# Performance work log

Measured on AMD Instinct MI355X. Metric: run time of the kernel, lower is better.

## Reference

```python
import jax, jax.numpy as jnp
import numpy as np

HEADS = 8

def _flatten(x, s1, s2):
    # 'b c (h s1) (w s2) -> b (h w) (s1 s2 c)'
    b, c, H, W = x.shape
    h, w = H // s1, W // s2
    x = x.reshape(b, c, h, s1, w, s2).transpose(0, 2, 4, 3, 5, 1)
    return x.reshape(b, h * w, s1 * s2 * c)

def _unflatten(x, h, w, s1, s2):
    # 'b (h w) (s1 s2 c) -> b c (h s1) (w s2)'
    b, n, e = x.shape
    c = e // (s1 * s2)
    x = x.reshape(b, h, w, s1, s2, c).transpose(0, 5, 1, 3, 2, 4)
    return x.reshape(b, c, h * s1, w * s2)

def _attn(x_detail, x_context, wq, bq, wk, bk, wv, bv, wo, bo):
    E = x_detail.shape[-1]
    d = E // HEADS
    scale = d ** -0.5
    def split(t):
        b, n, _ = t.shape
        return t.reshape(b, n, HEADS, d).transpose(0, 2, 1, 3)  # b h n d
    q = split(x_context @ wq.T + bq)
    k = split(x_detail @ wk.T + bk)
    v = split(x_detail @ wv.T + bv)
    att = jax.nn.softmax(jnp.einsum('bhqd,bhkd->bhqk', q, k) * scale, axis=-1)
    out = jnp.einsum('bhqk,bhkd->bhqd', att, v)
    b, h, n, _ = out.shape
    out = out.transpose(0, 2, 1, 3).reshape(b, n, E)
    return out @ wo.T + bo

def setup_inputs() -> dict:
    key = jax.random.key(0)
    ks = iter(jax.random.split(key, 64))
    inp = {}
    xshapes = [(16, 96, 56, 56), (16, 192, 28, 28), (16, 384, 14, 14), (16, 768, 7, 7)]
    names = ['x00', 'x10', 'x20', 'x30']
    for nm, sh in zip(names, xshapes):
        inp[nm + '_detail'] = jax.random.normal(next(ks), sh, dtype=jnp.float32)
        inp[nm + '_context'] = jax.random.normal(next(ks), sh, dtype=jnp.float32)
    embs = [384, 192, 384, 768]
    for i, E in enumerate(embs):
        for p in ['q', 'k', 'v', 'o']:
            inp[f'w{p}{i}'] = jax.random.normal(next(ks), (E, E), dtype=jnp.float32) * 0.02
            inp[f'b{p}{i}'] = jnp.zeros((E,), dtype=jnp.float32)
    return inp

def reference(x00_detail, x00_context, x10_detail, x10_context,
              x20_detail, x20_context, x30_detail, x30_context,
              wq0, bq0, wk0, bk0, wv0, bv0, wo0, bo0,
              wq1, bq1, wk1, bk1, wv1, bv1, wo1, bo1,
              wq2, bq2, wk2, bk2, wv2, bv2, wo2, bo2,
              wq3, bq3, wk3, bk3, wv3, bv3, wo3, bo3):
    # scale 0: 56x56 with 2x2 patching -> 784 tokens, emb 384
    o0 = x00_detail + _unflatten(
        _attn(_flatten(x00_detail, 2, 2), _flatten(x00_context, 2, 2),
              wq0, bq0, wk0, bk0, wv0, bv0, wo0, bo0), 28, 28, 2, 2)
    # scale 1: 28x28 -> 784 tokens, emb 192
    o1 = x10_detail + _unflatten(
        _attn(_flatten(x10_detail, 1, 1), _flatten(x10_context, 1, 1),
              wq1, bq1, wk1, bk1, wv1, bv1, wo1, bo1), 28, 28, 1, 1)
    # scale 2: 14x14 -> 196 tokens, emb 384
    o2 = x20_detail + _unflatten(
        _attn(_flatten(x20_detail, 1, 1), _flatten(x20_context, 1, 1),
              wq2, bq2, wk2, bk2, wv2, bv2, wo2, bo2), 14, 14, 1, 1)
    # scale 3: 7x7 -> 49 tokens, emb 768
    o3 = x30_detail + _unflatten(
        _attn(_flatten(x30_detail, 1, 1), _flatten(x30_context, 1, 1),
              wq3, bq3, wk3, bk3, wv3, bv3, wo3, bo3), 7, 7, 1, 1)
    return (o0, o1, o2, o3)
```

## Files before the change

### kernel.cpp

```cpp
#include <hip/hip_runtime.h>
#include <hip/hip_bf16.h>
#include <cstdint>
#include <cstddef>
#include <cmath>

typedef unsigned short bf16u;
typedef float f32x4 __attribute__((ext_vector_type(4)));
typedef short frag8 __attribute__((ext_vector_type(8)));

typedef __attribute__((address_space(1))) uint32_t u32g;
typedef __attribute__((address_space(3))) uint32_t u32l;

__device__ __forceinline__ void async_cp16(const bf16u* g, bf16u* l) {
    __builtin_amdgcn_global_load_lds((u32g*)g, (u32l*)l, 16, 0, 0);
}

__device__ __forceinline__ bf16u f2bf(float f) {
    union { float f; uint32_t u; } v; v.f = f;
    uint32_t u = v.u;
    return (bf16u)((u + 0x7fffu + ((u >> 16) & 1u)) >> 16);
}

__device__ __forceinline__ uint32_t pk2bf(float a, float b) {
    __hip_bfloat162 h = __float22bfloat162_rn(make_float2(a, b));
    union { __hip_bfloat162 h; uint32_t u; } c; c.h = h; return c.u;
}

__device__ __forceinline__ int vperm(int n) {
    return (n & ~63) | ((n & 15) << 2) | ((n >> 4) & 3);
}

static constexpr int cN[4]   = {784, 784, 196, 49};
static constexpr int cE[4]   = {384, 192, 384, 768};
static constexpr int cM[4]   = {12544, 12544, 3136, 784};
static constexpr int cC[4]   = {96, 192, 384, 768};
static constexpr int cH[4]   = {56, 28, 14, 7};
static constexpr int cS[4]   = {2, 1, 1, 1};
static constexpr int cWt[4]  = {28, 28, 14, 7};

static constexpr size_t xoff[4] = {0, 4816896, 7225344, 8429568};
static constexpr size_t voff[4] = {0, 6815744, 10223616, 12320768};
static constexpr size_t woff[4] = {0, 589824, 737280, 1327104};

__device__ __constant__ float qsc[4] = {0.20823509f, 0.29448888f, 0.20823509f, 0.14724444f};

static constexpr int hStart[5] = {0, 588, 735, 813, 1401};
static constexpr int oStart[5]  = {0,294,369,411,999};

static constexpr int fStart[9] = {0,4800,9600,12000,14400,15744,17088,17856,18624};
static constexpr int wCum[17]  = {0,72,144,216,288,306,324,342,360,432,504,576,648,936,1224,1512,1800};
static constexpr int fNtn[4] = {25, 25, 7, 2};
static constexpr int fNtc[4] = {3, 6, 12, 24};
static constexpr int fSp[4]  = {4, 1, 1, 1};

struct BiasP { const float* p[16]; };
struct PrepP { const float* x[8]; const float* w[16]; };
struct OunfP { const float* xd[4]; };

__global__ __launch_bounds__(256) void prep(PrepP pp, bf16u* __restrict__ Xd,
                                            bf16u* __restrict__ Xc, bf16u* __restrict__ Wb) {
    int blk = blockIdx.x, tid = threadIdx.x;
    if (blk < 18624) {
        __shared__ float tile[32][33];
        int seg = 0;
        while (seg < 7 && blk >= fStart[seg + 1]) seg++;
        int s = seg >> 1, which = seg & 1;
        int l = blk - fStart[seg];
        int ntn = fNtn[s], ntc = fNtc[s], sp = fSp[s];
        int nt = l % ntn; l /= ntn;
        int ctl = l % ntc; l /= ntc;
        int spi = l % sp; int b = l / sp;
        int sv = cS[s];
        int s1i = spi / sv, s2i = spi % sv;
        int C = cC[s], H = cH[s], Wd = cH[s], N = cN[s], E2 = cE[s], Wt = cWt[s];
        const float* x = pp.x[s * 2 + which];
        bf16u* dst = (which ? Xc : Xd) + xoff[s];
        int tx = tid & 31, ty = tid >> 5;
        int n0 = nt * 32, c0 = ctl * 32;
#pragma unroll
        for (int rr = 0; rr < 4; ++rr) {
            int c = c0 + rr * 8 + ty;
            int n = n0 + tx;
            if (n < N) {
                int hh = (n / Wt) * sv + s1i;
                int ww = (n % Wt) * sv + s2i;
                tile[rr * 8 + ty][tx] = x[((size_t)(b * C + c) * H + hh) * Wd + ww];
            }
        }
        __syncthreads();
        int ebase = (s1i * sv + s2i) * C + c0;
#pragma unroll
        for (int rr = 0; rr < 4; ++rr) {
            int n = n0 + rr * 8 + ty;
            if (n < N)
                dst[((size_t)b * N + n) * E2 + ebase + tx] = f2bf(tile[tx][rr * 8 + ty]);
        }
    } else {
        int wb = blk - 18624;
        int m2 = 0;
        while (m2 < 15 && wb >= wCum[m2 + 1]) m2++;
        int s = m2 >> 2, mi = m2 & 3;
        size_t e2 = (size_t)cE[s] * cE[s];
        size_t base = (size_t)(wb - wCum[m2]) * 2048 + tid * 8;
        const float* src = pp.w[m2];
        bf16u* dst = Wb + woff[s] + mi * e2 + base;
        float4 a = *(const float4*)(src + base);
        float4 c = *(const float4*)(src + base + 4);
        bf16u o[8] = {f2bf(a.x), f2bf(a.y), f2bf(a.z), f2bf(a.w),
                      f2bf(c.x), f2bf(c.y), f2bf(c.z), f2bf(c.w)};
        *(frag8*)dst = *(frag8*)o;
    }
}

__device__ __forceinline__ void gemm_q_h(const bf16u* __restrict__ A, const bf16u* __restrict__ W,
                                         const float* __restrict__ bias,
                                         int M, int E, int mTile, int eTile, float oscale,
                                         bf16u* __restrict__ outB, bf16u* sm) {
    bf16u* As = sm;
    bf16u* Bs = sm + 2048;
    int tid = threadIdx.x, wave = tid >> 6, lane = tid & 63;
    int mbase = mTile * 64, ebase = eTile * 128;
    int wm = (wave & 1) * 32, wn = (wave >> 1) * 64;
    f32x4 acc[2][4] = {};
    int srow = tid >> 2, sch = (tid & 3) * 8;
    int K = E;
    int m = mbase + srow; if (m >= M) m = M - 1;
    const bf16u* Ag  = A + (size_t)m * K + sch;
    const bf16u* Wg0 = W + (size_t)(ebase + srow) * K + sch;
    const bf16u* Wg1 = W + (size_t)(ebase + srow + 64) * K + sch;
    int la = (lane & 15) * 32 + (lane >> 4) * 8;

    for (int k0 = 0; k0 < K; k0 += 32) {
        async_cp16(Ag + k0, As + tid * 8);
        async_cp16(Wg0 + k0, Bs + tid * 8);
        async_cp16(Wg1 + k0, Bs + 2048 + tid * 8);
        __syncthreads();
        frag8 af[2], bfr[4];
#pragma unroll
        for (int i = 0; i < 2; ++i)
            af[i] = *(const frag8*)(As + (wm + i * 16) * 32 + la);
#pragma unroll
        for (int j = 0; j < 4; ++j)
            bfr[j] = *(const frag8*)(Bs + (wn + j * 16) * 32 + la);
#pragma unroll
        for (int i = 0; i < 2; ++i)
#pragma unroll
            for (int j = 0; j < 4; ++j)
                acc[i][j] = __builtin_amdgcn_mfma_f32_16x16x32_bf16(af[i], bfr[j], acc[i][j], 0, 0, 0);
        __syncthreads();
    }

    int mrow = lane & 15, quad = lane >> 4;
#pragma unroll
    for (int mt = 0; mt < 2; ++mt) {
#pragma unroll
        for (int nt = 0; nt < 4; ++nt) {
            int col = ebase + wn + nt * 16 + mrow;
            float bv = bias[col];
            int rbase = mbase + wm + mt * 16 + quad * 4;
#pragma unroll
            for (int r = 0; r < 4; ++r) {
                int rowg = rbase + r;
                if (rowg >= M) continue;
                outB[(size_t)rowg * E + col] = f2bf((acc[mt][nt][r] + bv) * oscale);
            }
        }
    }
}

template<int NN, int DHt, int DHPt, int NJt>
__device__ __forceinline__ void gemm_kv_h(const bf16u* __restrict__ A, const bf16u* __restrict__ Wk,
                                          const bf16u* __restrict__ Wv,
                                          const float* __restrict__ bk, const float* __restrict__ bv,
                                          int M, int E, int mTile, int eTile,
                                          bf16u* __restrict__ Ko, bf16u* __restrict__ Vo, bf16u* sm) {
    bf16u* As = sm;
    bf16u* Ks = sm + 2048;
    bf16u* Vs = sm + 6144;
    int tid = threadIdx.x, wave = tid >> 6, lane = tid & 63;
    int mbase = mTile * 64, ebase = eTile * 128;
    int wm = (wave & 1) * 32, wn = (wave >> 1) * 64;
    f32x4 acck[2][4] = {};
    f32x4 accv[2][4] = {};
    int srow = tid >> 2, sch = (tid & 3) * 8;
    int Kd = E;
    int m = mbase + srow; if (m >= M) m = M - 1;
    const bf16u* Ag  = A + (size_t)m * Kd + sch;
    const bf16u* Kg0 = Wk + (size_t)(ebase + srow) * Kd + sch;
    const bf16u* Kg1 = Wk + (size_t)(ebase + srow + 64) * Kd + sch;
    const bf16u* Vg0 = Wv + (size_t)(ebase + srow) * Kd + sch;
    const bf16u* Vg1 = Wv + (size_t)(ebase + srow + 64) * Kd + sch;
    int la = (lane & 15) * 32 + (lane >> 4) * 8;

    for (int k0 = 0; k0 < Kd; k0 += 32) {
        async_cp16(Ag + k0, As + tid * 8);
        async_cp16(Kg0 + k0, Ks + tid * 8);
        async_cp16(Kg1 + k0, Ks + 2048 + tid * 8);
        async_cp16(Vg0 + k0, Vs + tid * 8);
        async_cp16(Vg1 + k0, Vs + 2048 + tid * 8);
        __syncthreads();
        frag8 af[2], bfr[4];
#pragma unroll
        for (int i = 0; i < 2; ++i)
            af[i] = *(const frag8*)(As + (wm + i * 16) * 32 + la);
#pragma unroll
        for (int j = 0; j < 4; ++j)
            bfr[j] = *(const frag8*)(Ks + (wn + j * 16) * 32 + la);
#pragma unroll
        for (int i = 0; i < 2; ++i)
#pragma unroll
            for (int j = 0; j < 4; ++j)
                acck[i][j] = __builtin_amdgcn_mfma_f32_16x16x32_bf16(af[i], bfr[j], acck[i][j], 0, 0, 0);
#pragma unroll
        for (int j = 0; j < 4; ++j)
            bfr[j] = *(const frag8*)(Vs + (wn + j * 16) * 32 + la);
#pragma unroll
        for (int i = 0; i < 2; ++i)
#pragma unroll
            for (int j = 0; j < 4; ++j)
                accv[i][j] = __builtin_amdgcn_mfma_f32_16x16x32_bf16(af[i], bfr[j], accv[i][j], 0, 0, 0);
        __syncthreads();
    }

    int mrow = lane & 15, quad = lane >> 4;
#pragma unroll
    for (int mt = 0; mt < 2; ++mt) {
#pragma unroll
        for (int nt = 0; nt < 4; ++nt) {
            int col = ebase + wn + nt * 16 + mrow;
            float bkc = bk[col];
            int rbase = mbase + wm + mt * 16 + quad * 4;
#pragma unroll
            for (int r = 0; r < 4; ++r) {
                int rowg = rbase + r;
                if (rowg >= M) continue;
                Ko[(size_t)rowg * E + col] = f2bf(acck[mt][nt][r] + bkc);
            }
        }
    }

    bf16u* vt = sm;
#pragma unroll
    for (int mt = 0; mt < 2; ++mt) {
#pragma unroll
        for (int nt = 0; nt < 4; ++nt) {
            int cl = wn + nt * 16 + mrow;
            float bvc = bv[ebase + cl];
            int rl0 = wm + mt * 16 + quad * 4;
#pragma unroll
            for (int r = 0; r < 4; ++r)
                vt[cl * 66 + rl0 + r] = f2bf(accv[mt][nt][r] + bvc);
        }
    }
    __syncthreads();
    {
        int rowg = mbase + lane;
        bool ok = rowg < M;
        int b2 = rowg / NN, n = rowg - b2 * NN;
        int vp = vperm(n);
        int c0 = wave * 32;
#pragma unroll
        for (int ci = 0; ci < 32; ++ci) {
            int c = c0 + ci;
            int colg = ebase + c;
            int hh = colg / DHt, d = colg - hh * DHt;
            if (ok)
                Vo[((size_t)(b2 * 8 + hh) * DHPt + d) * NJt + vp] = vt[c * 66 + lane];
        }
    }
}

__device__ __forceinline__ void gemm_q64_s1(const bf16u* __restrict__ A, const bf16u* __restrict__ W,
                                            const float* __restrict__ bias,
                                            int M, int E, int mTile, int eTile, float oscale,
                                            bf16u* __restrict__ outB, bf16u* sm) {
    bf16u* As = sm;
    bf16u* Bs = sm + 2048;
    int tid = threadIdx.x, wave = tid >> 6, lane = tid & 63;
    int mbase = mTile * 64, ebase = eTile * 64;
    int wm = (wave & 1) * 32, wn = (wave >> 1) * 32;
    f32x4 acc[2][2] = {};
    int srow = tid >> 2, sch = (tid & 3) * 8;
    int K = E;
    int m = mbase + srow; if (m >= M) m = M - 1;
    const bf16u* Ag = A + (size_t)m * K + sch;
    const bf16u* Wg = W + (size_t)(ebase + srow) * K + sch;
    int la = (lane & 15) * 32 + (lane >> 4) * 8;

    for (int k0 = 0; k0 < K; k0 += 32) {
        async_cp16(Ag + k0, As + tid * 8);
        async_cp16(Wg + k0, Bs + tid * 8);
        __syncthreads();
        frag8 af0 = *(const frag8*)(As + wm * 32 + la);
        frag8 af1 = *(const frag8*)(As + (wm + 16) * 32 + la);
        frag8 bf0 = *(const frag8*)(Bs + wn * 32 + la);
        frag8 bf1 = *(const frag8*)(Bs + (wn + 16) * 32 + la);
        acc[0][0] = __builtin_amdgcn_mfma_f32_16x16x32_bf16(af0, bf0, acc[0][0], 0, 0, 0);
        acc[0][1] = __builtin_amdgcn_mfma_f32_16x16x32_bf16(af0, bf1, acc[0][1], 0, 0, 0);
        acc[1][0] = __builtin_amdgcn_mfma_f32_16x16x32_bf16(af1, bf0, acc[1][0], 0, 0, 0);
        acc[1][1] = __builtin_amdgcn_mfma_f32_16x16x32_bf16(af1, bf1, acc[1][1], 0, 0, 0);
        __syncthreads();
    }

    int mrow = lane & 15, quad = lane >> 4;
#pragma unroll
    for (int mt = 0; mt < 2; ++mt) {
#pragma unroll
        for (int nt = 0; nt < 2; ++nt) {
            int col = ebase + wn + nt * 16 + mrow;
            float bv = bias[col];
            int rbase = mbase + wm + mt * 16 + quad * 4;
#pragma unroll
            for (int r = 0; r < 4; ++r) {
                int rowg = rbase + r;
                if (rowg >= M) continue;
                outB[(size_t)rowg * E + col] = f2bf((acc[mt][nt][r] + bv) * oscale);
            }
        }
    }
}

template<int NN, int DHt, int DHPt, int NJt>
__device__ __forceinline__ void gemm_kv64(const bf16u* __restrict__ A, const bf16u* __restrict__ Wk,
                                          const bf16u* __restrict__ Wv,
                                          const float* __restrict__ bk, const float* __restrict__ bv,
                                          int M, int E, int mTile, int eTile,
                                          bf16u* __restrict__ Ko, bf16u* __restrict__ Vo, bf16u* sm) {
    bf16u* As = sm;
    bf16u* Ks = sm + 2048;
    bf16u* Vs = sm + 4096;
    int tid = threadIdx.x, wave = tid >> 6, lane = tid & 63;
    int mbase = mTile * 64, ebase = eTile * 64;
    int wm = (wave & 1) * 32, wn = (wave >> 1) * 32;
    f32x4 acck[2][2] = {};
    f32x4 accv[2][2] = {};
    int srow = tid >> 2, sch = (tid & 3) * 8;
    int Kd = E;
    int m = mbase + srow; if (m >= M) m = M - 1;
    const bf16u* Ag = A + (size_t)m * Kd + sch;
    const bf16u* Kg = Wk + (size_t)(ebase + srow) * Kd + sch;
    const bf16u* Vg = Wv + (size_t)(ebase + srow) * Kd + sch;
    int la = (lane & 15) * 32 + (lane >> 4) * 8;

    for (int k0 = 0; k0 < Kd; k0 += 32) {
        async_cp16(Ag + k0, As + tid * 8);
        async_cp16(Kg + k0, Ks + tid * 8);
        async_cp16(Vg + k0, Vs + tid * 8);
        __syncthreads();
        frag8 af0 = *(const frag8*)(As + wm * 32 + la);
        frag8 af1 = *(const frag8*)(As + (wm + 16) * 32 + la);
        frag8 k0f = *(const frag8*)(Ks + wn * 32 + la);
        frag8 k1f = *(const frag8*)(Ks + (wn + 16) * 32 + la);
        acck[0][0] = __builtin_amdgcn_mfma_f32_16x16x32_bf16(af0, k0f, acck[0][0], 0, 0, 0);
        acck[0][1] = __builtin_amdgcn_mfma_f32_16x16x32_bf16(af0, k1f, acck[0][1], 0, 0, 0);
        acck[1][0] = __builtin_amdgcn_mfma_f32_16x16x32_bf16(af1, k0f, acck[1][0], 0, 0, 0);
        acck[1][1] = __builtin_amdgcn_mfma_f32_16x16x32_bf16(af1, k1f, acck[1][1], 0, 0, 0);
        frag8 v0f = *(const frag8*)(Vs + wn * 32 + la);
        frag8 v1f = *(const frag8*)(Vs + (wn + 16) * 32 + la);
        accv[0][0] = __builtin_amdgcn_mfma_f32_16x16x32_bf16(af0, v0f, accv[0][0], 0, 0, 0);
        accv[0][1] = __builtin_amdgcn_mfma_f32_16x16x32_bf16(af0, v1f, accv[0][1], 0, 0, 0);
        accv[1][0] = __builtin_amdgcn_mfma_f32_16x16x32_bf16(af1, v0f, accv[1][0], 0, 0, 0);
        accv[1][1] = __builtin_amdgcn_mfma_f32_16x16x32_bf16(af1, v1f, accv[1][1], 0, 0, 0);
        __syncthreads();
    }

    int mrow = lane & 15, quad = lane >> 4;
#pragma unroll
    for (int mt = 0; mt < 2; ++mt) {
#pragma unroll
        for (int nt = 0; nt < 2; ++nt) {
            int col = ebase + wn + nt * 16 + mrow;
            float bkc = bk[col];
            int rbase = mbase + wm + mt * 16 + quad * 4;
#pragma unroll
            for (int r = 0; r < 4; ++r) {
                int rowg = rbase + r;
                if (rowg >= M) continue;
                Ko[(size_t)rowg * E + col] = f2bf(acck[mt][nt][r] + bkc);
            }
        }
    }

    bf16u* vt = sm;
#pragma unroll
    for (int mt = 0; mt < 2; ++mt) {
#pragma unroll
        for (int nt = 0; nt < 2; ++nt) {
            int cl = wn + nt * 16 + mrow;
            float bvc = bv[ebase + cl];
            int rl0 = wm + mt * 16 + quad * 4;
#pragma unroll
            for (int r = 0; r < 4; ++r)
                vt[cl * 66 + rl0 + r] = f2bf(accv[mt][nt][r] + bvc);
        }
    }
    __syncthreads();
    {
        int rowg = mbase + lane;
        bool ok = rowg < M;
        int b2 = rowg / NN, n = rowg - b2 * NN;
        int vp = vperm(n);
        int c0 = wave * 16;
#pragma unroll
        for (int ci = 0; ci < 16; ++ci) {
            int c = c0 + ci;
            int colg = ebase + c;
            int hh = colg / DHt, d = colg - hh * DHt;
            if (ok)
                Vo[((size_t)(b2 * 8 + hh) * DHPt + d) * NJt + vp] = vt[c * 66 + lane];
        }
    }
}

__global__ __launch_bounds__(256, 4) void qkv_all(const bf16u* __restrict__ Xd, const bf16u* __restrict__ Xc,
                                                  const bf16u* __restrict__ Wb,
                                                  bf16u* __restrict__ Qb, bf16u* __restrict__ Kb,
                                                  bf16u* __restrict__ Vt, BiasP bp) {
    __shared__ __align__(16) bf16u sm[10240];
    int blk0 = blockIdx.x;
    if (blk0 < 1401) {
        int blk = blk0;
        int seg = 0;
        while (seg < 3 && blk >= hStart[seg + 1]) seg++;
        int t = blk - hStart[seg];
        if (seg < 3) {
            int s = (seg == 0) ? 0 : (seg == 1 ? 2 : 3);
            int E = cE[s], M = cM[s];
            int ct = E >> 7;
            int mTile = t / ct, eTile = t - mTile * ct;
            const bf16u* A  = Xd + xoff[s];
            const bf16u* Wk = Wb + woff[s] + (size_t)1 * E * E;
            const bf16u* Wv = Wb + woff[s] + (size_t)2 * E * E;
            if (s == 0)
                gemm_kv_h<784, 48, 64, 832>(A, Wk, Wv, bp.p[1], bp.p[2], M, E, mTile, eTile,
                                            Kb + xoff[0], Vt + voff[0], sm);
            else if (s == 2)
                gemm_kv_h<196, 48, 64, 256>(A, Wk, Wv, bp.p[9], bp.p[10], M, E, mTile, eTile,
                                            Kb + xoff[2], Vt + voff[2], sm);
            else
                gemm_kv_h<49, 96, 96, 64>(A, Wk, Wv, bp.p[13], bp.p[14], M, E, mTile, eTile,
                                          Kb + xoff[3], Vt + voff[3], sm);
        } else {
            int E = 192, M = 12544;
            int mTile = t / 3, eTile = t - mTile * 3;
            gemm_kv64<784, 24, 32, 832>(Xd + xoff[1], Wb + woff[1] + (size_t)1 * E * E,
                                        Wb + woff[1] + (size_t)2 * E * E, bp.p[5], bp.p[6],
                                        M, E, mTile, eTile, Kb + xoff[1], Vt + voff[1], sm);
        }
    } else {
        int blk = blk0 - 1401;
        int seg = 0;
        while (seg < 3 && blk >= hStart[seg + 1]) seg++;
        int t = blk - hStart[seg];
        if (seg < 3) {
            int s = (seg == 0) ? 0 : (seg == 1 ? 2 : 3);
            int E = cE[s], M = cM[s];
            int ct = E >> 7;
            int mTile = t / ct, eTile = t - mTile * ct;
            gemm_q_h(Xc + xoff[s], Wb + woff[s], bp.p[s * 4], M, E, mTile, eTile,
                     qsc[s], Qb + xoff[s], sm);
        } else {
            int E = 192, M = 12544;
            int mTile = t / 3, eTile = t - mTile * 3;
            gemm_q64_s1(Xc + xoff[1], Wb + woff[1], bp.p[4], M, E, mTile, eTile,
                        qsc[1], Qb + xoff[1], sm);
        }
    }
}

__device__ __forceinline__ f32x4 bfly_add16(f32x4 v) {
#pragma unroll
    for (int m = 1; m <= 8; m <<= 1) {
        f32x4 o;
#pragma unroll
        for (int e = 0; e < 4; ++e) o[e] = __shfl_xor(v[e], m);
#pragma unroll
        for (int e = 0; e < 4; ++e) v[e] += o[e];
    }
    return v;
}

template<int DH, int N>
__device__ __forceinline__ void attn_body3(bf16u* __restrict__ smem,
                                           const bf16u* __restrict__ Q, const bf16u* __restrict__ K,
                                           const bf16u* __restrict__ Vt, bf16u* __restrict__ O,
                                           int lin) {
    constexpr int DHP = (DH == 24) ? 32 : 64;
    constexpr int C8  = DHP / 8;
    constexpr int CM  = C8 - 1;
    constexpr int KC  = DHP / 32;
    constexpr int DHT = (DH + 15) / 16;
    constexpr int VR  = DHT * 16;
    constexpr int NT  = (N + 63) / 64;
    constexpr int QT  = (N + 127) / 128;
    constexpr int NJc = NT * 64;
    constexpr int E   = DH * 8;
    constexpr int KS  = 64 * C8;
    constexpr int TS  = KS + VR * 8;
    constexpr int RND = (TS + 255) / 256;
    constexpr int PP  = 72;

    bf16u* buf0 = smem;
    bf16u* buf1 = smem + (size_t)TS * 8;
    bf16u* Ps   = smem + (size_t)2 * TS * 8;

    const int qt = lin % QT;
    const int r2 = lin / QT;
    const int h = r2 & 7, b = r2 >> 3;
    const int qb = qt * 128;
    const int tid = threadIdx.x, wave = tid >> 6, lane = tid & 63;
    const int mrow = lane & 15, quad = lane >> 4;

    const bf16u* Kb2 = K + (size_t)b * N * E + h * DH;
    const bf16u* Vb2 = Vt + (size_t)(b * 8 + h) * DHP * NJc;

    auto stage = [&](int jt, bf16u* buf) {
#pragma unroll
        for (int r = 0; r < RND; ++r) {
            int s = tid + r * 256;
            bf16u* dst = buf + (size_t)s * 8;
            if (s < KS) {
                int row = s / C8;
                int cl = (s & CM) ^ (row & CM);
                int n = jt * 64 + row; if (n >= N) n = N - 1;
                async_cp16(Kb2 + (size_t)n * E + cl * 8, dst);
            } else if (s < TS) {
                int v = s - KS;
                int d = v >> 3;
                int cl = (v & 7) ^ (d & 7);
                async_cp16(Vb2 + (size_t)d * NJc + jt * 64 + cl * 8, dst);
            }
        }
    };

    stage(0, buf0);

    frag8 qf0[KC], qf1[KC];
    {
        int qn0 = qb + wave * 32 + mrow;      if (qn0 >= N) qn0 = N - 1;
        int qn1 = qb + wave * 32 + 16 + mrow; if (qn1 >= N) qn1 = N - 1;
        const bf16u* qp0 = Q + (size_t)(b * N + qn0) * E + h * DH;
        const bf16u* qp1 = Q + (size_t)(b * N + qn1) * E + h * DH;
#pragma unroll
        for (int kc = 0; kc < KC; ++kc) {
            int col = kc * 32 + quad * 8;
            frag8 v0 = {}, v1 = {};
            if (col < DH) { v0 = *(const frag8*)(qp0 + col); v1 = *(const frag8*)(qp1 + col); }
            qf0[kc] = v0; qf1[kc] = v1;
        }
    }

    f32x4 lrun0 = {0.f, 0.f, 0.f, 0.f};
    f32x4 lrun1 = {0.f, 0.f, 0.f, 0.f};
    f32x4 oacc0[DHT], oacc1[DHT];
#pragma unroll
    for (int t = 0; t < DHT; ++t) { oacc0[t] = f32x4{0.f,0.f,0.f,0.f}; oacc1[t] = f32x4{0.f,0.f,0.f,0.f}; }

    bf16u* Pw = Ps + wave * 32 * PP;

    __syncthreads();

    int p = 0;
    for (int jt = 0; jt < NT; ++jt) {
        bf16u* KsB = p ? buf1 : buf0;
        bf16u* VsB = KsB + (size_t)KS * 8;
        if (jt + 1 < NT) stage(jt + 1, p ? buf0 : buf1);

        f32x4 s0[4], s1[4];
        const bool domask = ((N & 63) != 0) && (jt == NT - 1);
#pragma unroll
        for (int sub = 0; sub < 4; ++sub) {
            f32x4 a0 = {}, a1 = {};
#pragma unroll
            for (int kc = 0; kc < KC; ++kc) {
                int c = kc * 4 + quad;
                frag8 bfr = *(const frag8*)(KsB + ((size_t)((sub * 16 + mrow) * C8 + (c ^ (mrow & CM)))) * 8);
                a0 = __builtin_amdgcn_mfma_f32_16x16x32_bf16(qf0[kc], bfr, a0, 0, 0, 0);
                a1 = __builtin_amdgcn_mfma_f32_16x16x32_bf16(qf1[kc], bfr, a1, 0, 0, 0);
            }
            if (domask) {
                int col = jt * 64 + sub * 16 + mrow;
                if (col >= N) {
                    a0[0] = a0[1] = a0[2] = a0[3] = -30000.f;
                    a1[0] = a1[1] = a1[2] = a1[3] = -30000.f;
                }
            }
            s0[sub] = a0; s1[sub] = a1;
        }

#pragma unroll
        for (int sub = 0; sub < 4; ++sub)
#pragma unroll
            for (int e = 0; e < 4; ++e) {
                float p0 = __builtin_amdgcn_exp2f(s0[sub][e]);
                float p1 = __builtin_amdgcn_exp2f(s1[sub][e]);
                s0[sub][e] = p0; s1[sub][e] = p1;
                lrun0[e] += p0; lrun1[e] += p1;
            }

#pragma unroll
        for (int e = 0; e < 4; ++e) {
            uint2 u0, u1;
            u0.x = pk2bf(s0[0][e], s0[1][e]);
            u0.y = pk2bf(s0[2][e], s0[3][e]);
            u1.x = pk2bf(s1[0][e], s1[1][e]);
            u1.y = pk2bf(s1[2][e], s1[3][e]);
            *(uint2*)(Pw + (quad * 4 + e) * PP + mrow * 4) = u0;
            *(uint2*)(Pw + (16 + quad * 4 + e) * PP + mrow * 4) = u1;
        }

#pragma unroll
        for (int jc = 0; jc < 2; ++jc) {
            frag8 af0 = *(const frag8*)(Pw + mrow * PP + jc * 32 + quad * 8);
            frag8 af1 = *(const frag8*)(Pw + (16 + mrow) * PP + jc * 32 + quad * 8);
            int c = jc * 4 + quad;
#pragma unroll
            for (int t = 0; t < DHT; ++t) {
                frag8 bfr = *(const frag8*)(VsB + ((size_t)((t * 16 + mrow) * 8 + (c ^ (mrow & 7)))) * 8);
                oacc0[t] = __builtin_amdgcn_mfma_f32_16x16x32_bf16(af0, bfr, oacc0[t], 0, 0, 0);
                oacc1[t] = __builtin_amdgcn_mfma_f32_16x16x32_bf16(af1, bfr, oacc1[t], 0, 0, 0);
            }
        }
        __syncthreads();
        p ^= 1;
    }

    lrun0 = bfly_add16(lrun0);
    lrun1 = bfly_add16(lrun1);
    f32x4 linv0, linv1;
#pragma unroll
    for (int e = 0; e < 4; ++e) { linv0[e] = 1.0f / lrun0[e]; linv1[e] = 1.0f / lrun1[e]; }
#pragma unroll
    for (int t = 0; t < DHT; ++t) {
        int d = t * 16 + mrow;
        if (d >= DH) continue;
#pragma unroll
        for (int e = 0; e < 4; ++e) {
            int n0 = qb + wave * 32 + quad * 4 + e;
            int n1 = n0 + 16;
            if (n0 < N)
                O[((size_t)(b * N + n0)) * E + h * DH + d] = f2bf(oacc0[t][e] * linv0[e]);
            if (n1 < N)
                O[((size_t)(b * N + n1)) * E + h * DH + d] = f2bf(oacc1[t][e] * linv1[e]);
        }
    }
}

__device__ __forceinline__ void attn_s3_body(bf16u* __restrict__ smem,
                                             const bf16u* __restrict__ Qg, const bf16u* __restrict__ Kg,
                                             const bf16u* __restrict__ Vtg, bf16u* __restrict__ Og,
                                             int lin) {
    constexpr int DH = 96, N = 49, DHP = 96, KC = 3, DHT = 6, NJc = 64, E = 768;
    constexpr int KP = 104, QP = 104, VP = 72, PP = 72, C8 = 12;
    bf16u* Ks = smem;
    bf16u* Vs = Ks + 64 * KP;
    bf16u* QsPw = Vs + DHT * 16 * VP;

    const bf16u* Q = Qg + xoff[3];
    const bf16u* K = Kg + xoff[3];
    const bf16u* Vt = Vtg + voff[3];
    bf16u* O = Og + xoff[3];

    int h = lin & 7, b = lin >> 3;
    int tid = threadIdx.x, wave = tid >> 6, lane = tid & 63;
    int mrow = lane & 15, quad = lane >> 4;

    for (int idx = tid; idx < 64 * C8; idx += 256) {
        int row = idx / C8, col = (idx % C8) * 8;
        int n = row; if (n >= N) n = N - 1;
        frag8 v = {};
        if (col < DH) v = *(const frag8*)(Q + ((size_t)(b * N + n)) * E + h * DH + col);
        *(frag8*)(QsPw + row * QP + col) = v;
    }
    for (int idx = tid; idx < 64 * C8; idx += 256) {
        int row = idx / C8, col = (idx % C8) * 8;
        int n = row; if (n >= N) n = N - 1;
        frag8 v = {};
        if (col < DH) v = *(const frag8*)(K + (size_t)(b * N + n) * E + h * DH + col);
        *(frag8*)(Ks + row * KP + col) = v;
    }
    const bf16u* Vb2 = Vt + (size_t)(b * 8 + h) * DHP * NJc;
    for (int idx = tid; idx < DHT * 16 * 8; idx += 256) {
        int d = idx / 8, j = (idx % 8) * 8;
        frag8 v = {};
        if (d < DH) v = *(const frag8*)(Vb2 + (size_t)d * NJc + j);
        *(frag8*)(Vs + d * VP + j) = v;
    }
    __syncthreads();
    frag8 qf[KC];
#pragma unroll
    for (int kc = 0; kc < KC; ++kc)
        qf[kc] = *(const frag8*)(QsPw + (wave * 16 + mrow) * QP + kc * 32 + quad * 8);
    __syncthreads();
    bf16u* Pw = QsPw + wave * 16 * PP;

    f32x4 lrun = {0.f, 0.f, 0.f, 0.f};
    f32x4 oacc[DHT];
#pragma unroll
    for (int t = 0; t < DHT; ++t) oacc[t] = f32x4{0.f, 0.f, 0.f, 0.f};

    f32x4 s[4];
#pragma unroll
    for (int sub = 0; sub < 4; ++sub) {
        f32x4 acc = {};
#pragma unroll
        for (int kc = 0; kc < KC; ++kc) {
            frag8 bfr = *(const frag8*)(Ks + (sub * 16 + mrow) * KP + kc * 32 + quad * 8);
            acc = __builtin_amdgcn_mfma_f32_16x16x32_bf16(qf[kc], bfr, acc, 0, 0, 0);
        }
        int col = sub * 16 + mrow;
        if (col >= N) { acc[0] = acc[1] = acc[2] = acc[3] = -30000.f; }
        s[sub] = acc;
    }
#pragma unroll
    for (int sub = 0; sub < 4; ++sub)
#pragma unroll
        for (int e = 0; e < 4; ++e) {
            float px = __builtin_amdgcn_exp2f(s[sub][e]);
            s[sub][e] = px;
            lrun[e] += px;
        }
#pragma unroll
    for (int e = 0; e < 4; ++e) {
        uint2 u;
        u.x = pk2bf(s[0][e], s[1][e]);
        u.y = pk2bf(s[2][e], s[3][e]);
        *(uint2*)(Pw + (quad * 4 + e) * PP + mrow * 4) = u;
    }
#pragma unroll
    for (int jc = 0; jc < 2; ++jc) {
        frag8 af = *(const frag8*)(Pw + mrow * PP + jc * 32 + quad * 8);
#pragma unroll
        for (int t = 0; t < DHT; ++t) {
            frag8 bfr = *(const frag8*)(Vs + (t * 16 + mrow) * VP + jc * 32 + quad * 8);
            oacc[t] = __builtin_amdgcn_mfma_f32_16x16x32_bf16(af, bfr, oacc[t], 0, 0, 0);
        }
    }

    lrun = bfly_add16(lrun);
    f32x4 linv;
#pragma unroll
    for (int e = 0; e < 4; ++e) linv[e] = 1.0f / lrun[e];
#pragma unroll
    for (int t = 0; t < DHT; ++t) {
        int d = t * 16 + mrow;
#pragma unroll
        for (int e = 0; e < 4; ++e) {
            int n = wave * 16 + quad * 4 + e;
            if (n < N)
                O[((size_t)(b * N + n)) * E + h * DH + d] = f2bf(oacc[t][e] * linv[e]);
        }
    }
}

__global__ __launch_bounds__(256, 3) void attn_all(const bf16u* __restrict__ Qb, const bf16u* __restrict__ Kb,
                                                   const bf16u* __restrict__ Vt, bf16u* __restrict__ Ob) {
    __shared__ __align__(16) bf16u smem[23552];
    int g = blockIdx.x;
    if (g < 896) {
        int l = (g & 7) * 112 + (g >> 3);
        attn_body3<48, 784>(smem, Qb + xoff[0], Kb + xoff[0], Vt + voff[0], Ob + xoff[0], l);
    } else if (g < 1792) {
        int gg = g - 896;
        int l = (gg & 7) * 112 + (gg >> 3);
        attn_body3<24, 784>(smem, Qb + xoff[1], Kb + xoff[1], Vt + voff[1], Ob + xoff[1], l);
    } else if (g < 2048) {
        int gg = g - 1792;
        int l = (gg & 7) * 32 + (gg >> 3);
        attn_body3<48, 196>(smem, Qb + xoff[2], Kb + xoff[2], Vt + voff[2], Ob + xoff[2], l);
    } else {
        attn_s3_body(smem, Qb, Kb, Vt, Ob, g - 2048);
    }
}

template<int SC>
__device__ __forceinline__ size_t out_index(int rowg, int cg) {
    if (SC == 0) {
        int b = rowg / 784, n = rowg - b * 784;
        int slot = cg / 96, c = cg - slot * 96;
        int hh = n / 28, ww = n - hh * 28;
        return ((size_t)(b * 96 + c) * 56 + 2 * hh + (slot >> 1)) * 56 + 2 * ww + (slot & 1);
    } else if (SC == 1) {
        int b = rowg / 784, n = rowg - b * 784;
        return ((size_t)(b * 192 + cg)) * 784 + n;
    } else if (SC == 2) {
        int b = rowg / 196, n = rowg - b * 196;
        return ((size_t)(b * 384 + cg)) * 196 + n;
    } else {
        int b = rowg / 49, n = rowg - b * 49;
        return ((size_t)(b * 768 + cg)) * 49 + n;
    }
}

template<int SC>
__device__ __forceinline__ void o_tile128(const bf16u* __restrict__ A, const bf16u* __restrict__ W,
                                          const float* __restrict__ bias,
                                          const float* __restrict__ xd, float* __restrict__ out,
                                          int M, int E, int mTile, int eTile, bf16u* sm) {
    bf16u* A0 = sm;
    bf16u* B0 = sm + 4096;
    bf16u* A1 = sm + 8192;
    bf16u* B1 = sm + 12288;
    int tid = threadIdx.x, wave = tid >> 6, lane = tid & 63;
    int mbase = mTile * 128, ebase = eTile * 128;
    int wm = (wave & 1) * 64, wn = (wave >> 1) * 64;
    int mrow = lane & 15, quad = lane >> 4;
    f32x4 acc[4][4] = {};
    int srow = tid >> 2, sch = (tid & 3) * 8;
    int K = E;
    int m0 = mbase + srow;      if (m0 >= M) m0 = M - 1;
    int m1 = mbase + srow + 64; if (m1 >= M) m1 = M - 1;
    const bf16u* Ag0 = A + (size_t)m0 * K + sch;
    const bf16u* Ag1 = A + (size_t)m1 * K + sch;
    const bf16u* Wg0 = W + (size_t)(ebase + srow) * K + sch;
    const bf16u* Wg1 = W + (size_t)(ebase + srow + 64) * K + sch;
    int la = mrow * 32 + quad * 8;

    auto stage = [&](int k0, bf16u* As, bf16u* Bs) {
        async_cp16(Ag0 + k0, As + tid * 8);
        async_cp16(Ag1 + k0, As + 2048 + tid * 8);
        async_cp16(Wg0 + k0, Bs + tid * 8);
        async_cp16(Wg1 + k0, Bs + 2048 + tid * 8);
    };
    auto compute = [&](const bf16u* As, const bf16u* Bs) {
        frag8 af[4], bfr[4];
#pragma unroll
        for (int i = 0; i < 4; ++i) {
            af[i]  = *(const frag8*)(As + (wm + i * 16) * 32 + la);
            bfr[i] = *(const frag8*)(Bs + (wn + i * 16) * 32 + la);
        }
#pragma unroll
        for (int i = 0; i < 4; ++i)
#pragma unroll
            for (int j = 0; j < 4; ++j)
                acc[i][j] = __builtin_amdgcn_mfma_f32_16x16x32_bf16(af[i], bfr[j], acc[i][j], 0, 0, 0);
    };

    stage(0, A0, B0);
    __syncthreads();
    for (int k0 = 0; k0 < K; k0 += 64) {
        stage(k0 + 32, A1, B1);
        compute(A0, B0);
        __syncthreads();
        if (k0 + 64 < K) stage(k0 + 64, A0, B0);
        compute(A1, B1);
        if (k0 + 64 < K) __syncthreads();
    }

    float* Ls = (float*)sm;
#pragma unroll
    for (int ph = 0; ph < 4; ++ph) {
        __syncthreads();
        if ((wave & 1) == (ph >> 1)) {
            int mt0 = (ph & 1) * 2;
#pragma unroll
            for (int mi = 0; mi < 2; ++mi) {
                int mt = mt0 + mi;
#pragma unroll
                for (int nt = 0; nt < 4; ++nt)
#pragma unroll
                    for (int r = 0; r < 4; ++r)
                        Ls[(mi * 16 + quad * 4 + r) * 133 + wn + nt * 16 + mrow] = acc[mt][nt][r];
            }
        }
        __syncthreads();
        int rb = mbase + ph * 32;
#pragma unroll
        for (int i = 0; i < 16; ++i) {
            int coll = (tid >> 5) + i * 8;
            int l = tid & 31;
            int rg = rb + l;
            if (rg < M) {
                int cg = ebase + coll;
                size_t oi = out_index<SC>(rg, cg);
                out[oi] = xd[oi] + Ls[l * 133 + coll] + bias[cg];
            }
        }
    }
}

__device__ __forceinline__ void o_tile64_s1(const bf16u* __restrict__ A, const bf16u* __restrict__ W,
                                            const float* __restrict__ bias,
                                            const float* __restrict__ xd, float* __restrict__ out,
                                            int M, int E, int mTile, int eTile, bf16u* sm) {
    bf16u* A0 = sm;
    bf16u* B0 = sm + 2048;
    bf16u* A1 = sm + 4096;
    bf16u* B1 = sm + 6144;
    int tid = threadIdx.x, wave = tid >> 6, lane = tid & 63;
    int mbase = mTile * 64, ebase = eTile * 64;
    int wm = (wave & 1) * 32, wn = (wave >> 1) * 32;
    int mrow = lane & 15, quad = lane >> 4;
    f32x4 acc[2][2] = {};
    int srow = tid >> 2, sch = (tid & 3) * 8;
    int K = E;
    int m = mbase + srow; if (m >= M) m = M - 1;
    const bf16u* Ag = A + (size_t)m * K + sch;
    const bf16u* Wg = W + (size_t)(ebase + srow) * K + sch;
    int la = mrow * 32 + quad * 8;

    auto stage = [&](int k0, bf16u* As, bf16u* Bs) {
        async_cp16(Ag + k0, As + tid * 8);
        async_cp16(Wg + k0, Bs + tid * 8);
    };
    auto compute = [&](const bf16u* As, const bf16u* Bs) {
        frag8 af0 = *(const frag8*)(As + wm * 32 + la);
        frag8 af1 = *(const frag8*)(As + (wm + 16) * 32 + la);
        frag8 bf0 = *(const frag8*)(Bs + wn * 32 + la);
        frag8 bf1 = *(const frag8*)(Bs + (wn + 16) * 32 + la);
        acc[0][0] = __builtin_amdgcn_mfma_f32_16x16x32_bf16(af0, bf0, acc[0][0], 0, 0, 0);
        acc[0][1] = __builtin_amdgcn_mfma_f32_16x16x32_bf16(af0, bf1, acc[0][1], 0, 0, 0);
        acc[1][0] = __builtin_amdgcn_mfma_f32_16x16x32_bf16(af1, bf0, acc[1][0], 0, 0, 0);
        acc[1][1] = __builtin_amdgcn_mfma_f32_16x16x32_bf16(af1, bf1, acc[1][1], 0, 0, 0);
    };

    stage(0, A0, B0);
    __syncthreads();
    for (int k0 = 0; k0 < K; k0 += 64) {
        stage(k0 + 32, A1, B1);
        compute(A0, B0);
        __syncthreads();
        if (k0 + 64 < K) stage(k0 + 64, A0, B0);
        compute(A1, B1);
        if (k0 + 64 < K) __syncthreads();
    }

    float* Ls = (float*)sm;
#pragma unroll
    for (int ph = 0; ph < 2; ++ph) {
        __syncthreads();
        if ((wave & 1) == ph) {
#pragma unroll
            for (int mt = 0; mt < 2; ++mt)
#pragma unroll
                for (int nt = 0; nt < 2; ++nt)
#pragma unroll
                    for (int r = 0; r < 4; ++r)
                        Ls[(mt * 16 + quad * 4 + r) * 69 + wn + nt * 16 + mrow] = acc[mt][nt][r];
        }
        __syncthreads();
        int rb = mbase + ph * 32;
#pragma unroll
        for (int i = 0; i < 8; ++i) {
            int coll = (tid >> 5) + i * 8;
            int l = tid & 31;
            int rg = rb + l;
            if (rg < M) {
                int cg = ebase + coll;
                size_t oi = out_index<1>(rg, cg);
                out[oi] = xd[oi] + Ls[l * 69 + coll] + bias[cg];
            }
        }
    }
}

__global__ __launch_bounds__(256) void ounf_fat(const bf16u* __restrict__ Ob, const bf16u* __restrict__ Wb,
                                                float* __restrict__ out, BiasP bp, OunfP up) {
    __shared__ __align__(16) bf16u sm[16384];
    int blk = blockIdx.x;
    int seg = 0;
    while (seg < 3 && blk >= oStart[seg + 1]) seg++;
    int t = blk - oStart[seg];
    if (seg < 3) {
        int s = (seg == 0) ? 0 : (seg == 1 ? 2 : 3);
        int E = cE[s], M = cM[s];
        int ct = E >> 7;
        int mTile = t / ct, eTile = t - mTile * ct;
        const bf16u* A = Ob + xoff[s];
        const bf16u* W = Wb + woff[s] + (size_t)3 * E * E;
        if (s == 0)
            o_tile128<0>(A, W, bp.p[3], up.xd[0], out + xoff[0], M, E, mTile, eTile, sm);
        else if (s == 2)
            o_tile128<2>(A, W, bp.p[11], up.xd[2], out + xoff[2], M, E, mTile, eTile, sm);
        else
            o_tile128<3>(A, W, bp.p[15], up.xd[3], out + xoff[3], M, E, mTile, eTile, sm);
    } else {
        int E = 192, M = 12544;
        int mTile = t / 3, eTile = t - mTile * 3;
        o_tile64_s1(Ob + xoff[1], Wb + woff[1] + (size_t)3 * E * E, bp.p[7],
                    up.xd[1], out + xoff[1], M, E, mTile, eTile, sm);
    }
}

extern "C" void kernel_launch(void* const* d_in, const int* in_sizes, int n_in,
                              void* d_out, int out_size, void* d_ws, size_t ws_size,
                              hipStream_t stream) {
    bf16u* ws = (bf16u*)d_ws;
    bf16u* Qb = ws;
    bf16u* Kb = ws + 9031680;
    bf16u* Vt = ws + 18063360;
    bf16u* Ob = ws + 31170560;
    bf16u* Wb = ws + 40202240;
    bf16u* Xd = ws + 43888640;
    bf16u* Xc = ws + 52920320;
    float* out = (float*)d_out;

    PrepP pp; BiasP bb; OunfP ux;
    for (int s = 0; s < 4; ++s) {
        pp.x[s * 2]     = (const float*)d_in[s * 2];
        pp.x[s * 2 + 1] = (const float*)d_in[s * 2 + 1];
        ux.xd[s]        = (const float*)d_in[s * 2];
        int w0 = 8 + s * 8;
        pp.w[s * 4 + 0] = (const float*)d_in[w0 + 0];
        pp.w[s * 4 + 1] = (const float*)d_in[w0 + 2];
        pp.w[s * 4 + 2] = (const float*)d_in[w0 + 4];
        pp.w[s * 4 + 3] = (const float*)d_in[w0 + 6];
        bb.p[s * 4 + 0] = (const float*)d_in[w0 + 1];
        bb.p[s * 4 + 1] = (const float*)d_in[w0 + 3];
        bb.p[s * 4 + 2] = (const float*)d_in[w0 + 5];
        bb.p[s * 4 + 3] = (const float*)d_in[w0 + 7];
    }

    prep<<<20424, 256, 0, stream>>>(pp, Xd, Xc, Wb);
    qkv_all<<<2802, 256, 0, stream>>>(Xd, Xc, Wb, Qb, Kb, Vt, bb);
    attn_all<<<2176, 256, 0, stream>>>(Qb, Kb, Vt, Ob);
    ounf_fat<<<999, 256, 0, stream>>>(Ob, Wb, out, bb, ux);
}
```

Baseline: 353.4 us.

## Single-buffer attention K/V staging to raise occupancy, add MFMA priority hints

```diff
diff --git a/kernel.cpp b/kernel.cpp
--- a/kernel.cpp
+++ b/kernel.cpp
@@ -481,7 +481,7 @@
 }
 
 template<int DH, int N>
-__device__ __forceinline__ void attn_body3(bf16u* __restrict__ smem,
+__device__ __forceinline__ void attn_body4(bf16u* __restrict__ smem,
                                            const bf16u* __restrict__ Q, const bf16u* __restrict__ K,
                                            const bf16u* __restrict__ Vt, bf16u* __restrict__ O,
                                            int lin) {
@@ -500,9 +500,8 @@
     constexpr int RND = (TS + 255) / 256;
     constexpr int PP  = 72;
 
-    bf16u* buf0 = smem;
-    bf16u* buf1 = smem + (size_t)TS * 8;
-    bf16u* Ps   = smem + (size_t)2 * TS * 8;
+    bf16u* buf = smem;
+    bf16u* Ps  = smem + (size_t)TS * 8;
 
     const int qt = lin % QT;
     const int r2 = lin / QT;
@@ -514,7 +513,7 @@
     const bf16u* Kb2 = K + (size_t)b * N * E + h * DH;
     const bf16u* Vb2 = Vt + (size_t)(b * 8 + h) * DHP * NJc;
 
-    auto stage = [&](int jt, bf16u* buf) {
+    auto stage = [&](int jt) {
 #pragma unroll
         for (int r = 0; r < RND; ++r) {
             int s = tid + r * 256;
@@ -533,7 +532,7 @@
         }
     };
 
-    stage(0, buf0);
+    stage(0);
 
     frag8 qf0[KC], qf1[KC];
     {
@@ -558,16 +557,14 @@
 
     bf16u* Pw = Ps + wave * 32 * PP;
 
-    __syncthreads();
-
-    int p = 0;
     for (int jt = 0; jt < NT; ++jt) {
-        bf16u* KsB = p ? buf1 : buf0;
-        bf16u* VsB = KsB + (size_t)KS * 8;
-        if (jt + 1 < NT) stage(jt + 1, p ? buf0 : buf1);
+        __syncthreads();
+        bf16u* KsB = buf;
+        bf16u* VsB = buf + (size_t)KS * 8;
 
         f32x4 s0[4], s1[4];
         const bool domask = ((N & 63) != 0) && (jt == NT - 1);
+        __builtin_amdgcn_s_setprio(1);
 #pragma unroll
         for (int sub = 0; sub < 4; ++sub) {
             f32x4 a0 = {}, a1 = {};
@@ -587,6 +584,7 @@
             }
             s0[sub] = a0; s1[sub] = a1;
         }
+        __builtin_amdgcn_s_setprio(0);
 
 #pragma unroll
         for (int sub = 0; sub < 4; ++sub)
@@ -609,6 +607,7 @@
             *(uint2*)(Pw + (16 + quad * 4 + e) * PP + mrow * 4) = u1;
         }
 
+        __builtin_amdgcn_s_setprio(1);
 #pragma unroll
         for (int jc = 0; jc < 2; ++jc) {
             frag8 af0 = *(const frag8*)(Pw + mrow * PP + jc * 32 + quad * 8);
@@ -621,8 +620,10 @@
                 oacc1[t] = __builtin_amdgcn_mfma_f32_16x16x32_bf16(af1, bfr, oacc1[t], 0, 0, 0);
             }
         }
-        __syncthreads();
-        p ^= 1;
+        __builtin_amdgcn_s_setprio(0);
+
+        __syncthreads();
+        if (jt + 1 < NT) stage(jt + 1);
     }
 
     lrun0 = bfly_add16(lrun0);
@@ -650,12 +651,7 @@
                                              const bf16u* __restrict__ Qg, const bf16u* __restrict__ Kg,
                                              const bf16u* __restrict__ Vtg, bf16u* __restrict__ Og,
                                              int lin) {
-    constexpr int DH = 96, N = 49, DHP = 96, KC = 3, DHT = 6, NJc = 64, E = 768;
-    constexpr int KP = 104, QP = 104, VP = 72, PP = 72, C8 = 12;
-    bf16u* Ks = smem;
-    bf16u* Vs = Ks + 64 * KP;
-    bf16u* QsPw = Vs + DHT * 16 * VP;
-
+    constexpr int DH = 96, N = 49, DHP = 96, KC = 3, DHT = 6, NJc = 64, E = 768, PP = 72;
     const bf16u* Q = Qg + xoff[3];
     const bf16u* K = Kg + xoff[3];
     const bf16u* Vt = Vtg + voff[3];
@@ -665,34 +661,19 @@
     int tid = threadIdx.x, wave = tid >> 6, lane = tid & 63;
     int mrow = lane & 15, quad = lane >> 4;
 
-    for (int idx = tid; idx < 64 * C8; idx += 256) {
-        int row = idx / C8, col = (idx % C8) * 8;
-        int n = row; if (n >= N) n = N - 1;
-        frag8 v = {};
-        if (col < DH) v = *(const frag8*)(Q + ((size_t)(b * N + n)) * E + h * DH + col);
-        *(frag8*)(QsPw + row * QP + col) = v;
-    }
-    for (int idx = tid; idx < 64 * C8; idx += 256) {
-        int row = idx / C8, col = (idx % C8) * 8;
-        int n = row; if (n >= N) n = N - 1;
-        frag8 v = {};
-        if (col < DH) v = *(const frag8*)(K + (size_t)(b * N + n) * E + h * DH + col);
-        *(frag8*)(Ks + row * KP + col) = v;
-    }
+    const bf16u* Kb2 = K + (size_t)b * N * E + h * DH;
     const bf16u* Vb2 = Vt + (size_t)(b * 8 + h) * DHP * NJc;
-    for (int idx = tid; idx < DHT * 16 * 8; idx += 256) {
-        int d = idx / 8, j = (idx % 8) * 8;
-        frag8 v = {};
-        if (d < DH) v = *(const frag8*)(Vb2 + (size_t)d * NJc + j);
-        *(frag8*)(Vs + d * VP + j) = v;
-    }
-    __syncthreads();
+
     frag8 qf[KC];
-#pragma unroll
-    for (int kc = 0; kc < KC; ++kc)
-        qf[kc] = *(const frag8*)(QsPw + (wave * 16 + mrow) * QP + kc * 32 + quad * 8);
-    __syncthreads();
-    bf16u* Pw = QsPw + wave * 16 * PP;
+    {
+        int qn = wave * 16 + mrow; if (qn >= N) qn = N - 1;
+        const bf16u* qp = Q + (size_t)(b * N + qn) * E + h * DH;
+#pragma unroll
+        for (int kc = 0; kc < KC; ++kc)
+            qf[kc] = *(const frag8*)(qp + kc * 32 + quad * 8);
+    }
+
+    bf16u* Pw = smem + wave * 16 * PP;
 
     f32x4 lrun = {0.f, 0.f, 0.f, 0.f};
     f32x4 oacc[DHT];
@@ -700,18 +681,22 @@
     for (int t = 0; t < DHT; ++t) oacc[t] = f32x4{0.f, 0.f, 0.f, 0.f};
 
     f32x4 s[4];
+    __builtin_amdgcn_s_setprio(1);
 #pragma unroll
     for (int sub = 0; sub < 4; ++sub) {
         f32x4 acc = {};
+        int kr = sub * 16 + mrow; if (kr >= N) kr = N - 1;
+        const bf16u* kp = Kb2 + (size_t)kr * E;
 #pragma unroll
         for (int kc = 0; kc < KC; ++kc) {
-            frag8 bfr = *(const frag8*)(Ks + (sub * 16 + mrow) * KP + kc * 32 + quad * 8);
+            frag8 bfr = *(const frag8*)(kp + kc * 32 + quad * 8);
             acc = __builtin_amdgcn_mfma_f32_16x16x32_bf16(qf[kc], bfr, acc, 0, 0, 0);
         }
         int col = sub * 16 + mrow;
         if (col >= N) { acc[0] = acc[1] = acc[2] = acc[3] = -30000.f; }
         s[sub] = acc;
     }
+    __builtin_amdgcn_s_setprio(0);
 #pragma unroll
     for (int sub = 0; sub < 4; ++sub)
 #pragma unroll
@@ -727,15 +712,17 @@
         u.y = pk2bf(s[2][e], s[3][e]);
         *(uint2*)(Pw + (quad * 4 + e) * PP + mrow * 4) = u;
     }
+    __builtin_amdgcn_s_setprio(1);
 #pragma unroll
     for (int jc = 0; jc < 2; ++jc) {
         frag8 af = *(const frag8*)(Pw + mrow * PP + jc * 32 + quad * 8);
 #pragma unroll
         for (int t = 0; t < DHT; ++t) {
-            frag8 bfr = *(const frag8*)(Vs + (t * 16 + mrow) * VP + jc * 32 + quad * 8);
+            frag8 bfr = *(const frag8*)(Vb2 + (size_t)(t * 16 + mrow) * NJc + jc * 32 + quad * 8);
             oacc[t] = __builtin_amdgcn_mfma_f32_16x16x32_bf16(af, bfr, oacc[t], 0, 0, 0);
         }
     }
+    __builtin_amdgcn_s_setprio(0);
 
     lrun = bfly_add16(lrun);
     f32x4 linv;
@@ -753,21 +740,21 @@
     }
 }
 
-__global__ __launch_bounds__(256, 3) void attn_all(const bf16u* __restrict__ Qb, const bf16u* __restrict__ Kb,
+__global__ __launch_bounds__(256, 5) void attn_all(const bf16u* __restrict__ Qb, const bf16u* __restrict__ Kb,
                                                    const bf16u* __restrict__ Vt, bf16u* __restrict__ Ob) {
-    __shared__ __align__(16) bf16u smem[23552];
+    __shared__ __align__(16) bf16u smem[16384];
     int g = blockIdx.x;
     if (g < 896) {
         int l = (g & 7) * 112 + (g >> 3);
-        attn_body3<48, 784>(smem, Qb + xoff[0], Kb + xoff[0], Vt + voff[0], Ob + xoff[0], l);
+        attn_body4<48, 784>(smem, Qb + xoff[0], Kb + xoff[0], Vt + voff[0], Ob + xoff[0], l);
     } else if (g < 1792) {
         int gg = g - 896;
         int l = (gg & 7) * 112 + (gg >> 3);
-        attn_body3<24, 784>(smem, Qb + xoff[1], Kb + xoff[1], Vt + voff[1], Ob + xoff[1], l);
+        attn_body4<24, 784>(smem, Qb + xoff[1], Kb + xoff[1], Vt + voff[1], Ob + xoff[1], l);
     } else if (g < 2048) {
         int gg = g - 1792;
         int l = (gg & 7) * 32 + (gg >> 3);
-        attn_body3<48, 196>(smem, Qb + xoff[2], Kb + xoff[2], Vt + voff[2], Ob + xoff[2], l);
+        attn_body4<48, 196>(smem, Qb + xoff[2], Kb + xoff[2], Vt + voff[2], Ob + xoff[2], l);
     } else {
         attn_s3_body(smem, Qb, Kb, Vt, Ob, g - 2048);
     }
```

Result: slower. 440.6 us (+24.7%).
